# Kernel tuning notes

Hardware: AMD Instinct MI355X
Metric: run time of the kernel (lower is better)

The kernel has to match this reference:

```python
import jax, jax.numpy as jnp
import numpy as np

N_QUBIT = 20
N_LAYER = 50
FEAT = 128
BATCH = 128
N_NODES = BATCH * N_QUBIT * (N_LAYER + 1)  # 130560
N_EDGES = 524288
VOCAB = N_QUBIT * (N_LAYER + 1) + 1  # 1021
NEG_SLOPE = 0.01


def setup_inputs() -> dict:
    key = jax.random.key(0)
    ks = jax.random.split(key, 32)
    s = 0.05
    x = jax.random.randint(ks[0], (N_NODES,), 0, VOCAB, dtype=jnp.int64 if jax.config.read('jax_enable_x64') else jnp.int32)
    edge_index = jax.random.randint(ks[1], (2, N_EDGES), 0, N_NODES, dtype=x.dtype)
    emb = (jax.random.normal(ks[2], (VOCAB, FEAT), jnp.float32) * s).at[0].set(0.0)  # padding_idx=0
    gcn_w = jax.random.normal(ks[3], (5, FEAT, FEAT), jnp.float32) * s
    gcn_b = jnp.zeros((5, FEAT), jnp.float32)
    mlp_dims = [(2 * FEAT, 2 * FEAT), (2 * FEAT, FEAT), (FEAT, FEAT), (FEAT, FEAT // 2), (FEAT // 2, FEAT // 2), (FEAT // 2, 1)]
    mlp = {}
    for i, (din, dout) in enumerate(mlp_dims):
        mlp[f'mw{i}'] = jax.random.normal(ks[4 + i], (din, dout), jnp.float32) * s
        mlp[f'mb{i}'] = jnp.zeros((dout,), jnp.float32)
    return dict(x=x, edge_index=edge_index, emb=emb, gcn_w=gcn_w, gcn_b=gcn_b, **mlp)


def _leaky(v):
    return jnp.where(v >= 0, v, NEG_SLOPE * v)


def _gcn(h, src, dst, W, b):
    # PyG GCNConv: h' = D^-1/2 (A+I) D^-1/2 (h W) + b, flow src -> dst
    n = h.shape[0]
    hw = h @ W
    loops = jnp.arange(n, dtype=src.dtype)
    s2 = jnp.concatenate([src, loops])
    d2 = jnp.concatenate([dst, loops])
    deg = jax.ops.segment_sum(jnp.ones(s2.shape[0], hw.dtype), d2, num_segments=n)
    dinv = jnp.where(deg > 0, jax.lax.rsqrt(deg), 0.0)
    norm = dinv[s2] * dinv[d2]  # [E+N]
    out = jax.ops.segment_sum(hw[s2] * norm[:, None], d2, num_segments=n)
    return out + b


def reference(x, edge_index, emb, gcn_w, gcn_b, mw0, mb0, mw1, mb1, mw2, mb2, mw3, mb3, mw4, mb4, mw5, mb5):
    src, dst = edge_index[0], edge_index[1]
    h = emb[x]  # [N, f]
    for i in range(4):
        h = _leaky(_gcn(h, src, dst, gcn_w[i], gcn_b[i])) + h
    h = _gcn(h, src, dst, gcn_w[4], gcn_b[4]) + h
    n, f = N_QUBIT, FEAT
    h = h.reshape(-1, n * (N_LAYER + 1), f)[:, :n, :]  # [B, n, f]
    b = h.shape[0]
    # cartesian pairs (i, j): concat(h_i, h_j) -> [B, n, n, 2f]
    xi = jnp.broadcast_to(h[:, :, None, :], (b, n, n, f))
    xj = jnp.broadcast_to(h[:, None, :, :], (b, n, n, f))
    p = jnp.concatenate([xi, xj], axis=-1)
    p = _leaky(p @ mw0 + mb0)
    p = _leaky(p @ mw1 + mb1)
    p = _leaky(p @ mw2 + mb2)
    p = _leaky(p @ mw3 + mb3)
    p = _leaky(p @ mw4 + mb4)
    p = (p @ mw5 + mb5)[..., 0]  # [B, n, n]
    p = (p + jnp.swapaxes(p, -1, -2)) / 2
    return p.reshape(-1, n * n)
```

## Files before the change

kernel.cpp:

```cpp
#include <hip/hip_runtime.h>
#include <hip/hip_bf16.h>

#define NQ 20
#define NLAY 51
#define FEAT 128
#define BATCH 128
#define NN (BATCH * NQ * NLAY)
#define NE 524288
#define NPAIR (BATCH * NQ * NQ)
#define NB (NN / 256)
#define VOCAB 1021

typedef _Float16 half8 __attribute__((ext_vector_type(8)));
typedef float floatx4 __attribute__((ext_vector_type(4)));
typedef unsigned int uint;

__device__ __forceinline__ float lrelu(float v) { return v >= 0.f ? v : 0.01f * v; }

__device__ __forceinline__ uint packhl(float v) {
    _Float16 h = (_Float16)v;
    _Float16 l = (_Float16)(v - (float)h);
    union { _Float16 f; unsigned short u; } hb, lb;
    hb.f = h; lb.f = l;
    return (uint)hb.u | ((uint)lb.u << 16);
}

__device__ __forceinline__ void unpack8(uint4 a, uint4 b, half8& hi, half8& lo) {
    union { uint u[4]; half8 h; } H, L;
    H.u[0] = __builtin_amdgcn_perm(a.y, a.x, 0x05040100u);
    H.u[1] = __builtin_amdgcn_perm(a.w, a.z, 0x05040100u);
    H.u[2] = __builtin_amdgcn_perm(b.y, b.x, 0x05040100u);
    H.u[3] = __builtin_amdgcn_perm(b.w, b.z, 0x05040100u);
    L.u[0] = __builtin_amdgcn_perm(a.y, a.x, 0x07060302u);
    L.u[1] = __builtin_amdgcn_perm(a.w, a.z, 0x07060302u);
    L.u[2] = __builtin_amdgcn_perm(b.y, b.x, 0x07060302u);
    L.u[3] = __builtin_amdgcn_perm(b.w, b.z, 0x07060302u);
    hi = H.h;
    lo = L.h;
}

__global__ void k_count(const int* __restrict__ dst, int* __restrict__ cnt) {
    int e = blockIdx.x * 256 + threadIdx.x;
    atomicAdd(&cnt[dst[e]], 1);
}

__global__ void k_offsets(const int* __restrict__ cnt, const int* __restrict__ x,
                          int* __restrict__ offs, float* __restrict__ dinv,
                          int4* __restrict__ meta, int* __restrict__ cursor,
                          int* __restrict__ flag1, int* __restrict__ idmap) {
    __shared__ int sm[256];
    __shared__ int sbase;
    int t = threadIdx.x, g = blockIdx.x * 256 + t;
    int v = cnt[g];
    sm[t] = v;
    __syncthreads();
    for (int s = 1; s < 256; s <<= 1) {
        int add = (t >= s) ? sm[t - s] : 0;
        __syncthreads();
        sm[t] += add;
        __syncthreads();
    }
    if (t == 255) sbase = atomicAdd(cursor, sm[255]);
    __syncthreads();
    int off = sbase + sm[t] - v;
    float di = rsqrtf((float)(v + 1));
    offs[g] = off;
    dinv[g] = di;
    meta[g] = make_int4(off, v, __float_as_int(di), x[g]);
    if (g % (NQ * NLAY) < NQ) flag1[g] = 1;
    if (g < 1024) idmap[g] = min(g, VOCAB - 1);
}

__global__ void k_fill(const int* __restrict__ src, const int* __restrict__ dst,
                       const int* __restrict__ offs, int* __restrict__ fill,
                       const float* __restrict__ dinv, const int* __restrict__ x,
                       int2* __restrict__ csre, int2* __restrict__ csre0,
                       int* __restrict__ flag1) {
    int e = blockIdx.x * 256 + threadIdx.x;
    int d = dst[e];
    int s = src[e];
    int pos = offs[d] + atomicAdd(&fill[d], 1);
    int wb = __float_as_int(dinv[s] * dinv[d]);
    csre[pos] = make_int2(s, wb);
    csre0[pos] = make_int2(x[s], wb);
    if (d % (NQ * NLAY) < NQ) flag1[s] = 1;
}

__global__ void k_s1pass(const int* __restrict__ flagI, const int4* __restrict__ meta,
                         const int2* __restrict__ csre, int* __restrict__ cur,
                         int4* __restrict__ recO, int* __restrict__ flagO) {
    __shared__ int sm[256];
    __shared__ int sbase;
    int t = threadIdx.x, g = blockIdx.x * 256 + t;
    int v = flagI[g];
    sm[t] = v;
    __syncthreads();
    for (int s = 1; s < 256; s <<= 1) {
        int add = (t >= s) ? sm[t - s] : 0;
        __syncthreads();
        sm[t] += add;
        __syncthreads();
    }
    if (t == 255) sbase = atomicAdd(cur, sm[255]);
    __syncthreads();
    if (v) {
        int slot = sbase + sm[t] - 1;
        int4 m = meta[g];
        float di = __int_as_float(m.z);
        int dc = min(m.y, 6);
        int2 eb[6];
#pragma unroll
        for (int j = 0; j < 6; j++) eb[j] = (j < dc) ? csre[m.x + j] : make_int2(0, 0);
        int4* r = recO + (size_t)slot * 4;
        r[0] = make_int4(g + 1, m.y, __float_as_int(di * di), m.x);
        r[1] = make_int4(eb[0].x, eb[0].y, eb[1].x, eb[1].y);
        r[2] = make_int4(eb[2].x, eb[2].y, eb[3].x, eb[3].y);
        r[3] = make_int4(eb[4].x, eb[4].y, eb[5].x, eb[5].y);
        if (flagO) {
            flagO[g] = 1;
            for (int e = 0; e < m.y; e++) flagO[csre[m.x + e].x] = 1;
        }
    }
}

__global__ void k_rec0(const int4* __restrict__ meta, const int2* __restrict__ csre,
                       int4* __restrict__ rec0) {
    int q = blockIdx.x * 256 + threadIdx.x;
    if (q >= BATCH * NQ) return;
    int b = q / NQ, i = q - b * NQ;
    int node = b * (NQ * NLAY) + i;
    int4 m = meta[node];
    float di = __int_as_float(m.z);
    int dc = min(m.y, 6);
    int2 eb[6];
#pragma unroll
    for (int j = 0; j < 6; j++) eb[j] = (j < dc) ? csre[m.x + j] : make_int2(0, 0);
    int4* r = rec0 + (size_t)q * 4;
    r[0] = make_int4(node + 1, m.y, __float_as_int(di * di), m.x);
    r[1] = make_int4(eb[0].x, eb[0].y, eb[1].x, eb[1].y);
    r[2] = make_int4(eb[2].x, eb[2].y, eb[3].x, eb[3].y);
    r[3] = make_int4(eb[4].x, eb[4].y, eb[5].x, eb[5].y);
}

#define OFF_GCN 0
#define OFF_P0  81920
#define OFF_M1  147456
#define OFF_M2  180224
#define OFF_M3  196608
#define OFF_M4  204800
#define TS_TOTAL 208896

__global__ void k_tsplit_all(const float* __restrict__ gw, const float* __restrict__ mw0,
                             const float* __restrict__ mw1, const float* __restrict__ mw2,
                             const float* __restrict__ mw3, const float* __restrict__ mw4,
                             _Float16* __restrict__ hi, _Float16* __restrict__ lo) {
    int idx = blockIdx.x * 256 + threadIdx.x;
    const float* src;
    int K, N, rel;
    bool p0 = false;
    if (idx < OFF_P0) {
        int L = (idx - OFF_GCN) >> 14; rel = (idx - OFF_GCN) & 16383;
        src = gw + L * 16384; K = 128; N = 128;
    } else if (idx < OFF_M1) {
        rel = idx - OFF_P0; src = mw0; K = 128; N = 512; p0 = true;
    } else if (idx < OFF_M2) {
        rel = idx - OFF_M1;  src = mw1; K = 256; N = 128;
    } else if (idx < OFF_M3) {
        rel = idx - OFF_M2;  src = mw2; K = 128; N = 128;
    } else if (idx < OFF_M4) {
        rel = idx - OFF_M3;  src = mw3; K = 128; N = 64;
    } else {
        rel = idx - OFF_M4;  src = mw4; K = 64;  N = 64;
    }
    int kblks = K >> 5;
    int j = rel & 7;
    int lane = (rel >> 3) & 63;
    int t2 = rel >> 9;
    int kblk = t2 % kblks;
    int ntile = t2 / kblks;
    int col = ntile * 16 + (lane & 15);
    int k = kblk * 32 + ((lane >> 4) << 3) + j;
    float f;
    if (p0) {
        f = (col < 256) ? src[k * 256 + col] : src[(k + 128) * 256 + (col - 256)];
    } else {
        f = src[k * N + col];
    }
    _Float16 h = (_Float16)f;
    hi[idx] = h;
    lo[idx] = (_Float16)(f - (float)h);
}

template <int NT_N, bool LEAKY, bool BIAS, bool P0SPLIT, bool FUSEA, bool GATHA, bool LISTM>
__launch_bounds__(256, 2)
__global__ void hgemm(const float* __restrict__ A,
                      const float* __restrict__ FA, const float* __restrict__ FB,
                      const _Float16* __restrict__ Bh, const _Float16* __restrict__ Bl,
                      const float* __restrict__ bias,
                      float* __restrict__ C, float* __restrict__ C2,
                      int N, int K, const int* __restrict__ gmap,
                      const int* __restrict__ listm) {
    if (LISTM) {
        if ((unsigned)listm[blockIdx.x * 128] >= (unsigned)NN) return;
    }
    const int KB = K >> 5;
    const int lane = threadIdx.x & 63;
    const int wid = threadIdx.x >> 6;
    const int lm = lane & 15, lq = lane >> 4;
    const int m0 = blockIdx.x * 128 + wid * 32;
    const int n0t = blockIdx.y * NT_N;

    const float* arow[2];
    const float* brow[2];
#pragma unroll
    for (int mt = 0; mt < 2; mt++) {
        int row = m0 + mt * 16 + lm;
        if (FUSEA) {
            int b = row / (NQ * NQ);
            int rr = row - b * (NQ * NQ);
            int i = rr / NQ;
            int j = rr - i * NQ;
            arow[mt] = FA + (size_t)(b * NQ + i) * 256;
            brow[mt] = FB + (size_t)(b * NQ + j) * 256;
        } else if (GATHA) {
            arow[mt] = A + (size_t)gmap[row] * K;
        } else if (LISTM) {
            int lr = listm[row];
            lr = ((unsigned)lr < (unsigned)NN) ? lr : 0;
            arow[mt] = A + (size_t)lr * K;
        } else {
            arow[mt] = A + (size_t)row * K;
        }
    }

    floatx4 acc[2][NT_N];
#pragma unroll
    for (int mt = 0; mt < 2; mt++)
#pragma unroll
        for (int nt = 0; nt < NT_N; nt++) acc[mt][nt] = (floatx4)0.f;

    for (int kb = 0; kb < KB; kb++) {
        const int k0 = kb * 32 + lq * 8;
        half8 ahi[2], alo[2];
#pragma unroll
        for (int mt = 0; mt < 2; mt++) {
            floatx4 av0, av1;
            if (FUSEA) {
                floatx4 fa0 = *(const floatx4*)(arow[mt] + k0);
                floatx4 fa1 = *(const floatx4*)(arow[mt] + k0 + 4);
                floatx4 fb0 = *(const floatx4*)(brow[mt] + k0);
                floatx4 fb1 = *(const floatx4*)(brow[mt] + k0 + 4);
#pragma unroll
                for (int q = 0; q < 4; q++) {
                    av0[q] = lrelu(fa0[q] + fb0[q]);
                    av1[q] = lrelu(fa1[q] + fb1[q]);
                }
            } else {
                av0 = *(const floatx4*)(arow[mt] + k0);
                av1 = *(const floatx4*)(arow[mt] + k0 + 4);
            }
#pragma unroll
            for (int q = 0; q < 4; q++) {
                _Float16 h0 = (_Float16)av0[q];
                ahi[mt][q] = h0;
                alo[mt][q] = (_Float16)(av0[q] - (float)h0);
                _Float16 h1 = (_Float16)av1[q];
                ahi[mt][4 + q] = h1;
                alo[mt][4 + q] = (_Float16)(av1[q] - (float)h1);
            }
        }
#pragma unroll
        for (int nt = 0; nt < NT_N; nt++) {
            size_t boff = (((size_t)(n0t + nt) * KB + kb) * 64 + lane) * 8;
            half8 bhi = *(const half8*)(Bh + boff);
            half8 blo = *(const half8*)(Bl + boff);
#pragma unroll
            for (int mt = 0; mt < 2; mt++) {
                acc[mt][nt] = __builtin_amdgcn_mfma_f32_16x16x32_f16(ahi[mt], bhi, acc[mt][nt], 0, 0, 0);
                acc[mt][nt] = __builtin_amdgcn_mfma_f32_16x16x32_f16(ahi[mt], blo, acc[mt][nt], 0, 0, 0);
                acc[mt][nt] = __builtin_amdgcn_mfma_f32_16x16x32_f16(alo[mt], bhi, acc[mt][nt], 0, 0, 0);
            }
        }
    }

    int strow[2][4];
    bool svalid[2][4];
#pragma unroll
    for (int mt = 0; mt < 2; mt++)
#pragma unroll
        for (int r = 0; r < 4; r++) {
            int mlog = m0 + mt * 16 + lq * 4 + r;
            if (LISTM) {
                int sr = listm[mlog];
                svalid[mt][r] = (unsigned)sr < (unsigned)NN;
                strow[mt][r] = svalid[mt][r] ? sr : 0;
            } else {
                svalid[mt][r] = true;
                strow[mt][r] = mlog;
            }
        }

#pragma unroll
    for (int nt = 0; nt < NT_N; nt++) {
        int col = (n0t + nt) * 16 + lm;
        float bv = (BIAS || P0SPLIT) ? bias[col < 256 ? col : 0] : 0.f;
#pragma unroll
        for (int mt = 0; mt < 2; mt++) {
#pragma unroll
            for (int r = 0; r < 4; r++) {
                if (!svalid[mt][r]) continue;
                int row = strow[mt][r];
                float val = acc[mt][nt][r];
                if (P0SPLIT) {
                    if (col < 256) C[(size_t)row * 256 + col] = val + bv;
                    else C2[(size_t)row * 256 + col - 256] = val;
                } else {
                    if (BIAS) val += bv;
                    if (LEAKY) val = lrelu(val);
                    C[(size_t)row * N + col] = val;
                }
            }
        }
    }
}

template <bool LEAKY, bool FINAL>
__launch_bounds__(256, 8)
__global__ void k_lagg(const float* __restrict__ in, float* __restrict__ outp,
                       const int4* __restrict__ rec, const int2* __restrict__ csre,
                       const int* __restrict__ cntp, int fixcnt,
                       const _Float16* __restrict__ Bh, const _Float16* __restrict__ Bl,
                       const float* __restrict__ bias) {
    int lcnt = cntp ? *cntp : fixcnt;
    int sbase = blockIdx.x * 16;
    if (sbase >= lcnt) return;
    __shared__ uint X[16][132];
    __shared__ float R[16][132];
    __shared__ int NID[16];
    int tid = threadIdx.x;
    int sl = tid & 31;
    int grp = tid >> 5;
    const float4* in4 = (const float4*)in;
    {
        int lrow0 = grp * 2;
        int p0i = sbase + lrow0, p1i = p0i + 1;
        bool val0 = p0i < lcnt, val1 = p1i < lcnt;
        const int4* r0p = rec + (size_t)(val0 ? p0i : 0) * 4;
        const int4* r1p = rec + (size_t)(val1 ? p1i : 0) * 4;
        int4 hd0 = r0p[0], ea0 = r0p[1], eb0 = r0p[2], ec0 = r0p[3];
        int4 hd1 = r1p[0], ea1 = r1p[1], eb1 = r1p[2], ec1 = r1p[3];
        int n0 = hd0.x - 1;
        int n1 = hd1.x - 1;
        if (sl == 0) {
            NID[lrow0] = n0;
            NID[lrow0 + 1] = n1;
        }
        float s20 = __int_as_float(hd0.z), s21 = __int_as_float(hd1.z);
        float4 v0  = in4[(size_t)n0 * 32 + sl];
        float4 v1  = in4[(size_t)n1 * 32 + sl];
        float4 u00 = in4[(size_t)ea0.x * 32 + sl];
        float4 u01 = in4[(size_t)ea0.z * 32 + sl];
        float4 u02 = in4[(size_t)eb0.x * 32 + sl];
        float4 u03 = in4[(size_t)eb0.z * 32 + sl];
        float4 u04 = in4[(size_t)ec0.x * 32 + sl];
        float4 u05 = in4[(size_t)ec0.z * 32 + sl];
        float4 u10 = in4[(size_t)ea1.x * 32 + sl];
        float4 u11 = in4[(size_t)ea1.z * 32 + sl];
        float4 u12 = in4[(size_t)eb1.x * 32 + sl];
        float4 u13 = in4[(size_t)eb1.z * 32 + sl];
        float4 u14 = in4[(size_t)ec1.x * 32 + sl];
        float4 u15 = in4[(size_t)ec1.z * 32 + sl];
        *(float4*)&R[lrow0][sl * 4] = v0;
        *(float4*)&R[lrow0 + 1][sl * 4] = v1;
        float w00 = __int_as_float(ea0.y), w01 = __int_as_float(ea0.w);
        float w02 = __int_as_float(eb0.y), w03 = __int_as_float(eb0.w);
        float w04 = __int_as_float(ec0.y), w05 = __int_as_float(ec0.w);
        float w10 = __int_as_float(ea1.y), w11 = __int_as_float(ea1.w);
        float w12 = __int_as_float(eb1.y), w13 = __int_as_float(eb1.w);
        float w14 = __int_as_float(ec1.y), w15 = __int_as_float(ec1.w);
        float a0x = v0.x * s20 + u00.x * w00 + u01.x * w01 + u02.x * w02 + u03.x * w03 + u04.x * w04 + u05.x * w05;
        float a0y = v0.y * s20 + u00.y * w00 + u01.y * w01 + u02.y * w02 + u03.y * w03 + u04.y * w04 + u05.y * w05;
        float a0z = v0.z * s20 + u00.z * w00 + u01.z * w01 + u02.z * w02 + u03.z * w03 + u04.z * w04 + u05.z * w05;
        float a0w = v0.w * s20 + u00.w * w00 + u01.w * w01 + u02.w * w02 + u03.w * w03 + u04.w * w04 + u05.w * w05;
        float a1x = v1.x * s21 + u10.x * w10 + u11.x * w11 + u12.x * w12 + u13.x * w13 + u14.x * w14 + u15.x * w15;
        float a1y = v1.y * s21 + u10.y * w10 + u11.y * w11 + u12.y * w12 + u13.y * w13 + u14.y * w14 + u15.y * w15;
        float a1z = v1.z * s21 + u10.z * w10 + u11.z * w11 + u12.z * w12 + u13.z * w13 + u14.z * w14 + u15.z * w15;
        float a1w = v1.w * s21 + u10.w * w10 + u11.w * w11 + u12.w * w12 + u13.w * w13 + u14.w * w14 + u15.w * w15;
        int deg0 = val0 ? hd0.y : 0, deg1 = val1 ? hd1.y : 0;
        int dm = max(deg0, deg1);
        if (dm > 6) {
            int off0 = hd0.w, off1 = hd1.w;
            int d0c = max(deg0 - 1, 0), d1c = max(deg1 - 1, 0);
            for (int e = 6; e < dm; e += 6) {
                int2 e00 = csre[off0 + min(e,     d0c)];
                int2 e01 = csre[off0 + min(e + 1, d0c)];
                int2 e02 = csre[off0 + min(e + 2, d0c)];
                int2 e03 = csre[off0 + min(e + 3, d0c)];
                int2 e04 = csre[off0 + min(e + 4, d0c)];
                int2 e05 = csre[off0 + min(e + 5, d0c)];
                int2 e10 = csre[off1 + min(e,     d1c)];
                int2 e11 = csre[off1 + min(e + 1, d1c)];
                int2 e12 = csre[off1 + min(e + 2, d1c)];
                int2 e13 = csre[off1 + min(e + 3, d1c)];
                int2 e14 = csre[off1 + min(e + 4, d1c)];
                int2 e15 = csre[off1 + min(e + 5, d1c)];
                float4 x00 = in4[(size_t)e00.x * 32 + sl];
                float4 x01 = in4[(size_t)e01.x * 32 + sl];
                float4 x02 = in4[(size_t)e02.x * 32 + sl];
                float4 x03 = in4[(size_t)e03.x * 32 + sl];
                float4 x04 = in4[(size_t)e04.x * 32 + sl];
                float4 x05 = in4[(size_t)e05.x * 32 + sl];
                float4 x10 = in4[(size_t)e10.x * 32 + sl];
                float4 x11 = in4[(size_t)e11.x * 32 + sl];
                float4 x12 = in4[(size_t)e12.x * 32 + sl];
                float4 x13 = in4[(size_t)e13.x * 32 + sl];
                float4 x14 = in4[(size_t)e14.x * 32 + sl];
                float4 x15 = in4[(size_t)e15.x * 32 + sl];
                float q00 = (e     < deg0) ? __int_as_float(e00.y) : 0.f;
                float q01 = (e + 1 < deg0) ? __int_as_float(e01.y) : 0.f;
                float q02 = (e + 2 < deg0) ? __int_as_float(e02.y) : 0.f;
                float q03 = (e + 3 < deg0) ? __int_as_float(e03.y) : 0.f;
                float q04 = (e + 4 < deg0) ? __int_as_float(e04.y) : 0.f;
                float q05 = (e + 5 < deg0) ? __int_as_float(e05.y) : 0.f;
                float q10 = (e     < deg1) ? __int_as_float(e10.y) : 0.f;
                float q11 = (e + 1 < deg1) ? __int_as_float(e11.y) : 0.f;
                float q12 = (e + 2 < deg1) ? __int_as_float(e12.y) : 0.f;
                float q13 = (e + 3 < deg1) ? __int_as_float(e13.y) : 0.f;
                float q14 = (e + 4 < deg1) ? __int_as_float(e14.y) : 0.f;
                float q15 = (e + 5 < deg1) ? __int_as_float(e15.y) : 0.f;
                a0x += x00.x * q00 + x01.x * q01 + x02.x * q02 + x03.x * q03 + x04.x * q04 + x05.x * q05;
                a0y += x00.y * q00 + x01.y * q01 + x02.y * q02 + x03.y * q03 + x04.y * q04 + x05.y * q05;
                a0z += x00.z * q00 + x01.z * q01 + x02.z * q02 + x03.z * q03 + x04.z * q04 + x05.z * q05;
                a0w += x00.w * q00 + x01.w * q01 + x02.w * q02 + x03.w * q03 + x04.w * q04 + x05.w * q05;
                a1x += x10.x * q10 + x11.x * q11 + x12.x * q12 + x13.x * q13 + x14.x * q14 + x15.x * q15;
                a1y += x10.y * q10 + x11.y * q11 + x12.y * q12 + x13.y * q13 + x14.y * q14 + x15.y * q15;
                a1z += x10.z * q10 + x11.z * q11 + x12.z * q12 + x13.z * q13 + x14.z * q14 + x15.z * q15;
                a1w += x10.w * q10 + x11.w * q11 + x12.w * q12 + x13.w * q13 + x14.w * q14 + x15.w * q15;
            }
        }
        *(uint4*)&X[lrow0][sl * 4] =
            make_uint4(packhl(a0x), packhl(a0y), packhl(a0z), packhl(a0w));
        *(uint4*)&X[lrow0 + 1][sl * 4] =
            make_uint4(packhl(a1x), packhl(a1y), packhl(a1z), packhl(a1w));
    }
    __syncthreads();
    const int lane = tid & 63;
    const int wid = tid >> 6;
    const int lm = lane & 15, lq = lane >> 4;
    floatx4 acc[2];
    acc[0] = (floatx4)0.f;
    acc[1] = (floatx4)0.f;
#pragma unroll
    for (int kb = 0; kb < 4; kb++) {
        const int k0 = kb * 32 + lq * 8;
        uint4 pa = *(const uint4*)&X[lm][k0];
        uint4 pb = *(const uint4*)&X[lm][k0 + 4];
        half8 ahi, alo;
        unpack8(pa, pb, ahi, alo);
#pragma unroll
        for (int ntl = 0; ntl < 2; ntl++) {
            int nt = wid * 2 + ntl;
            size_t boff = (((size_t)nt * 4 + kb) * 64 + lane) * 8;
            half8 bhi = *(const half8*)(Bh + boff);
            half8 blo = *(const half8*)(Bl + boff);
            acc[ntl] = __builtin_amdgcn_mfma_f32_16x16x32_f16(ahi, bhi, acc[ntl], 0, 0, 0);
            acc[ntl] = __builtin_amdgcn_mfma_f32_16x16x32_f16(ahi, blo, acc[ntl], 0, 0, 0);
            acc[ntl] = __builtin_amdgcn_mfma_f32_16x16x32_f16(alo, bhi, acc[ntl], 0, 0, 0);
        }
    }
    int nodes[4];
    bool sval[4];
#pragma unroll
    for (int r = 0; r < 4; r++) {
        int slot = sbase + lq * 4 + r;
        sval[r] = slot < lcnt;
        nodes[r] = NID[lq * 4 + r];
    }
#pragma unroll
    for (int ntl = 0; ntl < 2; ntl++) {
        int col = (wid * 2 + ntl) * 16 + lm;
        float bv = bias[col];
#pragma unroll
        for (int r = 0; r < 4; r++) {
            if (!sval[r]) continue;
            float val = acc[ntl][r] + bv;
            if (LEAKY) val = lrelu(val);
            val += R[lq * 4 + r][col];
            if (FINAL)
                outp[(size_t)(sbase + lq * 4 + r) * FEAT + col] = val;
            else
                outp[(size_t)nodes[r] * FEAT + col] = val;
        }
    }
}

template <int KB, int NT>
__device__ __forceinline__ void pair_stage(uint (*__restrict__ X)[132],
                                           const _Float16* __restrict__ Bh,
                                           const _Float16* __restrict__ Bl,
                                           const float* __restrict__ bias,
                                           int srow, int lane) {
    const int lm = lane & 15, lq = lane >> 4;
    floatx4 acc[NT];
#pragma unroll
    for (int nt = 0; nt < NT; nt++) acc[nt] = (floatx4)0.f;
#pragma unroll
    for (int kb = 0; kb < KB; kb++) {
        const int k0 = kb * 32 + lq * 8;
        uint4 pa = *(const uint4*)&X[srow + lm][k0];
        uint4 pb = *(const uint4*)&X[srow + lm][k0 + 4];
        half8 ahi, alo;
        unpack8(pa, pb, ahi, alo);
#pragma unroll
        for (int nt = 0; nt < NT; nt++) {
            size_t boff = (((size_t)nt * KB + kb) * 64 + lane) * 8;
            half8 bhi = *(const half8*)(Bh + boff);
            half8 blo = *(const half8*)(Bl + boff);
            acc[nt] = __builtin_amdgcn_mfma_f32_16x16x32_f16(ahi, bhi, acc[nt], 0, 0, 0);
            acc[nt] = __builtin_amdgcn_mfma_f32_16x16x32_f16(ahi, blo, acc[nt], 0, 0, 0);
            acc[nt] = __builtin_amdgcn_mfma_f32_16x16x32_f16(alo, bhi, acc[nt], 0, 0, 0);
        }
    }
#pragma unroll
    for (int nt = 0; nt < NT; nt++) {
        int col = nt * 16 + lm;
        float bv = bias[col];
#pragma unroll
        for (int r = 0; r < 4; r++) {
            X[srow + lq * 4 + r][col] = packhl(lrelu(acc[nt][r] + bv));
        }
    }
}

__launch_bounds__(256, 4)
__global__ void k_pair(const float* __restrict__ FA, const float* __restrict__ FB,
                       const _Float16* __restrict__ bth, const _Float16* __restrict__ btl,
                       const float* __restrict__ mb1, const float* __restrict__ mb2,
                       const float* __restrict__ mb3, const float* __restrict__ mb4,
                       const float* __restrict__ mw5, const float* __restrict__ mb5,
                       float* __restrict__ sbuf) {
    __shared__ uint X[64][132];
    const int lane = threadIdx.x & 63;
    const int wid = threadIdx.x >> 6;
    const int lm = lane & 15, lq = lane >> 4;
    const int srow = wid * 16;
    const int rbase = blockIdx.x * 64;

    {
        const int grow = rbase + srow + lm;
        int b = grow / (NQ * NQ);
        int rr = grow - b * (NQ * NQ);
        int i = rr / NQ;
        int j = rr - i * NQ;
        const float* arow = FA + (size_t)(b * NQ + i) * 256;
        const float* brow = FB + (size_t)(b * NQ + j) * 256;
        const _Float16* Bh = bth + OFF_M1;
        const _Float16* Bl = btl + OFF_M1;
        floatx4 acc[8];
#pragma unroll
        for (int nt = 0; nt < 8; nt++) acc[nt] = (floatx4)0.f;
        const int KB = 8;
#pragma unroll
        for (int kb = 0; kb < KB; kb++) {
            const int k0 = kb * 32 + lq * 8;
            floatx4 fa0 = *(const floatx4*)(arow + k0);
            floatx4 fa1 = *(const floatx4*)(arow + k0 + 4);
            floatx4 fb0 = *(const floatx4*)(brow + k0);
            floatx4 fb1 = *(const floatx4*)(brow + k0 + 4);
            half8 ahi, alo;
#pragma unroll
            for (int q = 0; q < 4; q++) {
                float v0 = lrelu(fa0[q] + fb0[q]);
                float v1 = lrelu(fa1[q] + fb1[q]);
                _Float16 h0 = (_Float16)v0;
                ahi[q] = h0;
                alo[q] = (_Float16)(v0 - (float)h0);
                _Float16 h1 = (_Float16)v1;
                ahi[4 + q] = h1;
                alo[4 + q] = (_Float16)(v1 - (float)h1);
            }
#pragma unroll
            for (int nt = 0; nt < 8; nt++) {
                size_t boff = (((size_t)nt * KB + kb) * 64 + lane) * 8;
                half8 bhi = *(const half8*)(Bh + boff);
                half8 blo = *(const half8*)(Bl + boff);
                acc[nt] = __builtin_amdgcn_mfma_f32_16x16x32_f16(ahi, bhi, acc[nt], 0, 0, 0);
                acc[nt] = __builtin_amdgcn_mfma_f32_16x16x32_f16(ahi, blo, acc[nt], 0, 0, 0);
                acc[nt] = __builtin_amdgcn_mfma_f32_16x16x32_f16(alo, bhi, acc[nt], 0, 0, 0);
            }
        }
#pragma unroll
        for (int nt = 0; nt < 8; nt++) {
            int col = nt * 16 + lm;
            float bv = mb1[col];
#pragma unroll
            for (int r = 0; r < 4; r++) {
                X[srow + lq * 4 + r][col] = packhl(lrelu(acc[nt][r] + bv));
            }
        }
    }
    pair_stage<4, 8>(X, bth + OFF_M2, btl + OFF_M2, mb2, srow, lane);
    pair_stage<4, 4>(X, bth + OFF_M3, btl + OFF_M3, mb3, srow, lane);
    pair_stage<2, 4>(X, bth + OFF_M4, btl + OFF_M4, mb4, srow, lane);
    {
        int row = srow + (lane >> 2);
        int part = lane & 3;
        float s = 0.f;
#pragma unroll
        for (int c4 = 0; c4 < 4; c4++) {
            int c0 = part * 16 + c4 * 4;
            uint4 u = *(const uint4*)&X[row][c0];
            const float* wp = mw5 + c0;
            uint uu[4] = {u.x, u.y, u.z, u.w};
#pragma unroll
            for (int q = 0; q < 4; q++) {
                union { unsigned short us; _Float16 f; } ch, cl;
                ch.us = (unsigned short)(uu[q] & 0xffffu);
                cl.us = (unsigned short)(uu[q] >> 16);
                s += ((float)ch.f + (float)cl.f) * wp[q];
            }
        }
        s += __shfl_xor(s, 1);
        s += __shfl_xor(s, 2);
        if (part == 0) sbuf[rbase + row] = s + mb5[0];
    }
}

__global__ void k_sym(const float* __restrict__ sbuf, float* __restrict__ out) {
    int p = blockIdx.x * 256 + threadIdx.x;
    int b = p / (NQ * NQ);
    int rr = p - b * (NQ * NQ);
    int i = rr / NQ, j = rr - i * NQ;
    float a = sbuf[p];
    float c = sbuf[b * (NQ * NQ) + j * NQ + i];
    out[p] = 0.5f * (a + c);
}

__global__ void k_agg0(const float* __restrict__ embW, const float* __restrict__ emb,
                       float* __restrict__ h,
                       const int4* __restrict__ meta, const int2* __restrict__ csre0,
                       const float* __restrict__ bias) {
    int tid = threadIdx.x;
    int sl = tid & 31;
    int p = blockIdx.x * 8 + (tid >> 5);
    int n0 = p * 2, n1 = n0 + 1;
    int4 m0 = meta[n0], m1 = meta[n1];
    float di0 = __int_as_float(m0.z), di1 = __int_as_float(m1.z);
    int off0 = m0.x, deg0 = m0.y;
    int off1 = m1.x, deg1 = m1.y;
    float4 v0 = ((const float4*)(embW + (size_t)m0.w * FEAT))[sl];
    float4 v1 = ((const float4*)(embW + (size_t)m1.w * FEAT))[sl];
    float4 ho0 = ((const float4*)(emb + (size_t)m0.w * FEAT))[sl];
    float4 ho1 = ((const float4*)(emb + (size_t)m1.w * FEAT))[sl];
    float s20 = di0 * di0, s21 = di1 * di1;
    float a0x = v0.x * s20, a0y = v0.y * s20, a0z = v0.z * s20, a0w = v0.w * s20;
    float a1x = v1.x * s21, a1y = v1.y * s21, a1z = v1.z * s21, a1w = v1.w * s21;
    int d0c = max(deg0 - 1, 0), d1c = max(deg1 - 1, 0);
    int dm = max(deg0, deg1);
    for (int e = 0; e < dm; e += 4) {
        int2 e00 = csre0[off0 + min(e,     d0c)];
        int2 e01 = csre0[off0 + min(e + 1, d0c)];
        int2 e02 = csre0[off0 + min(e + 2, d0c)];
        int2 e03 = csre0[off0 + min(e + 3, d0c)];
        int2 e10 = csre0[off1 + min(e,     d1c)];
        int2 e11 = csre0[off1 + min(e + 1, d1c)];
        int2 e12 = csre0[off1 + min(e + 2, d1c)];
        int2 e13 = csre0[off1 + min(e + 3, d1c)];
        float4 u00 = ((const float4*)(embW + (size_t)e00.x * FEAT))[sl];
        float4 u01 = ((const float4*)(embW + (size_t)e01.x * FEAT))[sl];
        float4 u02 = ((const float4*)(embW + (size_t)e02.x * FEAT))[sl];
        float4 u03 = ((const float4*)(embW + (size_t)e03.x * FEAT))[sl];
        float4 u10 = ((const float4*)(embW + (size_t)e10.x * FEAT))[sl];
        float4 u11 = ((const float4*)(embW + (size_t)e11.x * FEAT))[sl];
        float4 u12 = ((const float4*)(embW + (size_t)e12.x * FEAT))[sl];
        float4 u13 = ((const float4*)(embW + (size_t)e13.x * FEAT))[sl];
        float w00 = (e     < deg0) ? __int_as_float(e00.y) : 0.f;
        float w01 = (e + 1 < deg0) ? __int_as_float(e01.y) : 0.f;
        float w02 = (e + 2 < deg0) ? __int_as_float(e02.y) : 0.f;
        float w03 = (e + 3 < deg0) ? __int_as_float(e03.y) : 0.f;
        float w10 = (e     < deg1) ? __int_as_float(e10.y) : 0.f;
        float w11 = (e + 1 < deg1) ? __int_as_float(e11.y) : 0.f;
        float w12 = (e + 2 < deg1) ? __int_as_float(e12.y) : 0.f;
        float w13 = (e + 3 < deg1) ? __int_as_float(e13.y) : 0.f;
        a0x += u00.x * w00 + u01.x * w01 + u02.x * w02 + u03.x * w03;
        a0y += u00.y * w00 + u01.y * w01 + u02.y * w02 + u03.y * w03;
        a0z += u00.z * w00 + u01.z * w01 + u02.z * w02 + u03.z * w03;
        a0w += u00.w * w00 + u01.w * w01 + u02.w * w02 + u03.w * w03;
        a1x += u10.x * w10 + u11.x * w11 + u12.x * w12 + u13.x * w13;
        a1y += u10.y * w10 + u11.y * w11 + u12.y * w12 + u13.y * w13;
        a1z += u10.z * w10 + u11.z * w11 + u12.z * w12 + u13.z * w13;
        a1w += u10.w * w10 + u11.w * w11 + u12.w * w12 + u13.w * w13;
    }
    float4 bv = ((const float4*)bias)[sl];
    float4 r0, r1;
    r0.x = lrelu(a0x + bv.x) + ho0.x;
    r0.y = lrelu(a0y + bv.y) + ho0.y;
    r0.z = lrelu(a0z + bv.z) + ho0.z;
    r0.w = lrelu(a0w + bv.w) + ho0.w;
    r1.x = lrelu(a1x + bv.x) + ho1.x;
    r1.y = lrelu(a1y + bv.y) + ho1.y;
    r1.z = lrelu(a1z + bv.z) + ho1.z;
    r1.w = lrelu(a1w + bv.w) + ho1.w;
    ((float4*)(h + (size_t)n0 * FEAT))[sl] = r0;
    ((float4*)(h + (size_t)n1 * FEAT))[sl] = r1;
}

extern "C" void kernel_launch(void* const* d_in, const int* in_sizes, int n_in,
                              void* d_out, int out_size, void* d_ws, size_t ws_size,
                              hipStream_t stream) {
    const int* x = (const int*)d_in[0];
    const int* ei = (const int*)d_in[1];
    const int* e_src = ei;
    const int* e_dst = ei + NE;
    const float* emb = (const float*)d_in[2];
    const float* gw = (const float*)d_in[3];
    const float* gb = (const float*)d_in[4];
    const float* mw0 = (const float*)d_in[5];
    const float* mb0 = (const float*)d_in[6];
    const float* mw1 = (const float*)d_in[7];
    const float* mb1 = (const float*)d_in[8];
    const float* mw2 = (const float*)d_in[9];
    const float* mb2 = (const float*)d_in[10];
    const float* mw3 = (const float*)d_in[11];
    const float* mb3 = (const float*)d_in[12];
    const float* mw4 = (const float*)d_in[13];
    const float* mb4 = (const float*)d_in[14];
    const float* mw5 = (const float*)d_in[15];
    const float* mb5 = (const float*)d_in[16];
    float* out = (float*)d_out;

    float* wsf = (float*)d_ws;
    size_t o = 0;
    const size_t HSZ = (size_t)NN * FEAT;
    float* h  = wsf + o; o += HSZ;
    float* hw = wsf + o; o += HSZ;
    int* cnt   = (int*)(wsf + o); o += NN;
    int* fill  = (int*)(wsf + o); o += NN;
    int* flag1 = (int*)(wsf + o); o += NN;
    int* flag2 = (int*)(wsf + o); o += NN;
    int* flag3 = (int*)(wsf + o); o += NN;
    int* curs  = (int*)(wsf + o); o += 16;
    int* offs = (int*)(wsf + o); o += NN;
    float* dinv = wsf + o; o += NN;
    int4* meta = (int4*)(wsf + o); o += 4 * (size_t)NN;
    int2* csre  = (int2*)(wsf + o); o += 2 * (size_t)(NE + 8);
    int2* csre0 = (int2*)(wsf + o); o += 2 * (size_t)(NE + 8);
    int* idmap = (int*)(wsf + o); o += 1024;
    float* embW = wsf + o; o += (size_t)1024 * FEAT;
    float* hq = wsf + o; o += (size_t)BATCH * NQ * FEAT;
    float* Abuf = wsf + o; o += (size_t)BATCH * NQ * 256;
    float* Bbuf = wsf + o; o += (size_t)BATCH * NQ * 256;
    int4* rec1 = (int4*)(wsf + o); o += 16 * (size_t)NN;
    int4* rec2 = (int4*)(wsf + o); o += 16 * (size_t)NN;
    int4* rec3 = (int4*)(wsf + o); o += 16 * (size_t)NN;
    int4* rec0 = (int4*)(wsf + o); o += 16 * (size_t)(BATCH * NQ);
    _Float16* bt_hi = (_Float16*)(wsf + o); o += (TS_TOTAL + 2) / 2;
    _Float16* bt_lo = (_Float16*)(wsf + o); o += (TS_TOTAL + 2) / 2;
    float* sbuf = hw;

    k_tsplit_all<<<TS_TOTAL / 256, 256, 0, stream>>>(gw, mw0, mw1, mw2, mw3, mw4, bt_hi, bt_lo);

    hipMemsetAsync(cnt, 0, (5 * NN + 16) * sizeof(int), stream);
    hipMemsetAsync(csre + NE, 0, 8 * sizeof(int2), stream);
    hipMemsetAsync(csre0 + NE, 0, 8 * sizeof(int2), stream);
    k_count<<<NE / 256, 256, 0, stream>>>(e_dst, cnt);
    k_offsets<<<NB, 256, 0, stream>>>(cnt, x, offs, dinv, meta, curs + 0, flag1, idmap);
    k_fill<<<NE / 256, 256, 0, stream>>>(e_src, e_dst, offs, fill, dinv, x, csre, csre0, flag1);
    k_rec0<<<(BATCH * NQ + 255) / 256, 256, 0, stream>>>(meta, csre, rec0);
    k_s1pass<<<NB, 256, 0, stream>>>(flag1, meta, csre, curs + 1, rec1, flag2);
    k_s1pass<<<NB, 256, 0, stream>>>(flag2, meta, csre, curs + 2, rec2, flag3);
    k_s1pass<<<NB, 256, 0, stream>>>(flag3, meta, csre, curs + 3, rec3, nullptr);

    hgemm<1, false, false, false, false, true, false><<<dim3(8, 8), 256, 0, stream>>>(
        emb, nullptr, nullptr, bt_hi + OFF_GCN, bt_lo + OFF_GCN,
        nullptr, embW, nullptr, FEAT, FEAT, idmap, nullptr);
    k_agg0<<<NN / 16, 256, 0, stream>>>(embW, emb, h, meta, csre0, gb + 0 * FEAT);

    k_lagg<true, false><<<NN / 16, 256, 0, stream>>>(
        h, hw, rec3, csre, curs + 3, 0,
        bt_hi + OFF_GCN + 1 * 16384, bt_lo + OFF_GCN + 1 * 16384, gb + 1 * FEAT);
    k_lagg<true, false><<<NN / 16, 256, 0, stream>>>(
        hw, h, rec2, csre, curs + 2, 0,
        bt_hi + OFF_GCN + 2 * 16384, bt_lo + OFF_GCN + 2 * 16384, gb + 2 * FEAT);
    k_lagg<true, false><<<NN / 16, 256, 0, stream>>>(
        h, hw, rec1, csre, curs + 1, 0,
        bt_hi + OFF_GCN + 3 * 16384, bt_lo + OFF_GCN + 3 * 16384, gb + 3 * FEAT);
    k_lagg<false, true><<<(BATCH * NQ) / 16, 256, 0, stream>>>(
        hw, hq, rec0, csre, nullptr, BATCH * NQ,
        bt_hi + OFF_GCN + 4 * 16384, bt_lo + OFF_GCN + 4 * 16384, gb + 4 * FEAT);

    hgemm<2, false, false, true, false, false, false><<<dim3(20, 16), 256, 0, stream>>>(
        hq, nullptr, nullptr, bt_hi + OFF_P0, bt_lo + OFF_P0, mb0, Abuf, Bbuf, 512, 128,
        nullptr, nullptr);
    k_pair<<<NPAIR / 64, 256, 0, stream>>>(Abuf, Bbuf, bt_hi, bt_lo,
                                           mb1, mb2, mb3, mb4, mw5, mb5, sbuf);
    k_sym<<<NPAIR / 256, 256, 0, stream>>>(sbuf, out);
}
```

Measured before the change: 390.1 us.

## Fuse rec0 build, pair-projection GEMM and symmetrization into neighbouring kernels

Folds the rec0 record construction into the first k_s1pass launch as extra blocks. Fuses the final GCN layer with the first MLP projection (hq @ mw0 split into A/B halves), keeping the tile in shared memory. Replaces k_sym with atomic adds from k_pair into a zeroed output. This removes three launches and the hq/sbuf round trips, at the cost of an output memset and two atomics per pair.

```diff
diff --git a/kernel.cpp b/kernel.cpp
--- a/kernel.cpp
+++ b/kernel.cpp
@@ -88,7 +88,27 @@
 
 __global__ void k_s1pass(const int* __restrict__ flagI, const int4* __restrict__ meta,
                          const int2* __restrict__ csre, int* __restrict__ cur,
-                         int4* __restrict__ recO, int* __restrict__ flagO) {
+                         int4* __restrict__ recO, int* __restrict__ flagO,
+                         int4* __restrict__ rec0q) {
+    if (rec0q && blockIdx.x >= NB) {
+        int q = (blockIdx.x - NB) * 256 + threadIdx.x;
+        if (q < BATCH * NQ) {
+            int b = q / NQ, i = q - b * NQ;
+            int node = b * (NQ * NLAY) + i;
+            int4 m = meta[node];
+            float di = __int_as_float(m.z);
+            int dc = min(m.y, 6);
+            int2 eb[6];
+#pragma unroll
+            for (int j = 0; j < 6; j++) eb[j] = (j < dc) ? csre[m.x + j] : make_int2(0, 0);
+            int4* r = rec0q + (size_t)q * 4;
+            r[0] = make_int4(node + 1, m.y, __float_as_int(di * di), m.x);
+            r[1] = make_int4(eb[0].x, eb[0].y, eb[1].x, eb[1].y);
+            r[2] = make_int4(eb[2].x, eb[2].y, eb[3].x, eb[3].y);
+            r[3] = make_int4(eb[4].x, eb[4].y, eb[5].x, eb[5].y);
+        }
+        return;
+    }
     __shared__ int sm[256];
     __shared__ int sbase;
     int t = threadIdx.x, g = blockIdx.x * 256 + t;
@@ -121,25 +141,6 @@
             for (int e = 0; e < m.y; e++) flagO[csre[m.x + e].x] = 1;
         }
     }
-}
-
-__global__ void k_rec0(const int4* __restrict__ meta, const int2* __restrict__ csre,
-                       int4* __restrict__ rec0) {
-    int q = blockIdx.x * 256 + threadIdx.x;
-    if (q >= BATCH * NQ) return;
-    int b = q / NQ, i = q - b * NQ;
-    int node = b * (NQ * NLAY) + i;
-    int4 m = meta[node];
-    float di = __int_as_float(m.z);
-    int dc = min(m.y, 6);
-    int2 eb[6];
-#pragma unroll
-    for (int j = 0; j < 6; j++) eb[j] = (j < dc) ? csre[m.x + j] : make_int2(0, 0);
-    int4* r = rec0 + (size_t)q * 4;
-    r[0] = make_int4(node + 1, m.y, __float_as_int(di * di), m.x);
-    r[1] = make_int4(eb[0].x, eb[0].y, eb[1].x, eb[1].y);
-    r[2] = make_int4(eb[2].x, eb[2].y, eb[3].x, eb[3].y);
-    r[3] = make_int4(eb[4].x, eb[4].y, eb[5].x, eb[5].y);
 }
 
 #define OFF_GCN 0
@@ -330,7 +331,10 @@
                        const int4* __restrict__ rec, const int2* __restrict__ csre,
                        const int* __restrict__ cntp, int fixcnt,
                        const _Float16* __restrict__ Bh, const _Float16* __restrict__ Bl,
-                       const float* __restrict__ bias) {
+                       const float* __restrict__ bias,
+                       const _Float16* __restrict__ BhP, const _Float16* __restrict__ BlP,
+                       const float* __restrict__ mb0p,
+                       float* __restrict__ Abuf, float* __restrict__ Bbuf) {
     int lcnt = cntp ? *cntp : fixcnt;
     int sbase = blockIdx.x * 16;
     if (sbase >= lcnt) return;
@@ -468,6 +472,7 @@
             acc[ntl] = __builtin_amdgcn_mfma_f32_16x16x32_f16(alo, bhi, acc[ntl], 0, 0, 0);
         }
     }
+    if (FINAL) __syncthreads();
     int nodes[4];
     bool sval[4];
 #pragma unroll
@@ -487,9 +492,48 @@
             if (LEAKY) val = lrelu(val);
             val += R[lq * 4 + r][col];
             if (FINAL)
-                outp[(size_t)(sbase + lq * 4 + r) * FEAT + col] = val;
+                X[lq * 4 + r][col] = packhl(val);
             else
                 outp[(size_t)nodes[r] * FEAT + col] = val;
+        }
+    }
+    if (FINAL) {
+        __syncthreads();
+#pragma unroll
+        for (int c = 0; c < 2; c++) {
+            floatx4 acc4[4];
+#pragma unroll
+            for (int nt = 0; nt < 4; nt++) acc4[nt] = (floatx4)0.f;
+#pragma unroll
+            for (int kb = 0; kb < 4; kb++) {
+                const int k0 = kb * 32 + lq * 8;
+                uint4 pa = *(const uint4*)&X[lm][k0];
+                uint4 pb = *(const uint4*)&X[lm][k0 + 4];
+                half8 ahi, alo;
+                unpack8(pa, pb, ahi, alo);
+#pragma unroll
+                for (int nt = 0; nt < 4; nt++) {
+                    int T = wid * 8 + c * 4 + nt;
+                    size_t boff = (((size_t)T * 4 + kb) * 64 + lane) * 8;
+                    half8 bhi = *(const half8*)(BhP + boff);
+                    half8 blo = *(const half8*)(BlP + boff);
+                    acc4[nt] = __builtin_amdgcn_mfma_f32_16x16x32_f16(ahi, bhi, acc4[nt], 0, 0, 0);
+                    acc4[nt] = __builtin_amdgcn_mfma_f32_16x16x32_f16(ahi, blo, acc4[nt], 0, 0, 0);
+                    acc4[nt] = __builtin_amdgcn_mfma_f32_16x16x32_f16(alo, bhi, acc4[nt], 0, 0, 0);
+                }
+            }
+#pragma unroll
+            for (int nt = 0; nt < 4; nt++) {
+                int T = wid * 8 + c * 4 + nt;
+                int col = T * 16 + lm;
+#pragma unroll
+                for (int r = 0; r < 4; r++) {
+                    int q = sbase + lq * 4 + r;
+                    float val = acc4[nt][r];
+                    if (col < 256) Abuf[(size_t)q * 256 + col] = val + mb0p[col];
+                    else Bbuf[(size_t)q * 256 + col - 256] = val;
+                }
+            }
         }
     }
 }
@@ -538,7 +582,7 @@
                        const float* __restrict__ mb1, const float* __restrict__ mb2,
                        const float* __restrict__ mb3, const float* __restrict__ mb4,
                        const float* __restrict__ mw5, const float* __restrict__ mb5,
-                       float* __restrict__ sbuf) {
+                       float* __restrict__ out) {
     __shared__ uint X[64][132];
     const int lane = threadIdx.x & 63;
     const int wid = threadIdx.x >> 6;
@@ -622,18 +666,16 @@
         }
         s += __shfl_xor(s, 1);
         s += __shfl_xor(s, 2);
-        if (part == 0) sbuf[rbase + row] = s + mb5[0];
-    }
-}
-
-__global__ void k_sym(const float* __restrict__ sbuf, float* __restrict__ out) {
-    int p = blockIdx.x * 256 + threadIdx.x;
-    int b = p / (NQ * NQ);
-    int rr = p - b * (NQ * NQ);
-    int i = rr / NQ, j = rr - i * NQ;
-    float a = sbuf[p];
-    float c = sbuf[b * (NQ * NQ) + j * NQ + i];
-    out[p] = 0.5f * (a + c);
+        if (part == 0) {
+            int p = rbase + row;
+            int b = p / (NQ * NQ);
+            int rr = p - b * (NQ * NQ);
+            int i = rr / NQ, j = rr - i * NQ;
+            float hv = 0.5f * (s + mb5[0]);
+            atomicAdd(&out[(size_t)b * NQ * NQ + i * NQ + j], hv);
+            atomicAdd(&out[(size_t)b * NQ * NQ + j * NQ + i], hv);
+        }
+    }
 }
 
 __global__ void k_agg0(const float* __restrict__ embW, const float* __restrict__ emb,
@@ -747,7 +789,6 @@
     int2* csre0 = (int2*)(wsf + o); o += 2 * (size_t)(NE + 8);
     int* idmap = (int*)(wsf + o); o += 1024;
     float* embW = wsf + o; o += (size_t)1024 * FEAT;
-    float* hq = wsf + o; o += (size_t)BATCH * NQ * FEAT;
     float* Abuf = wsf + o; o += (size_t)BATCH * NQ * 256;
     float* Bbuf = wsf + o; o += (size_t)BATCH * NQ * 256;
     int4* rec1 = (int4*)(wsf + o); o += 16 * (size_t)NN;
@@ -756,7 +797,8 @@
     int4* rec0 = (int4*)(wsf + o); o += 16 * (size_t)(BATCH * NQ);
     _Float16* bt_hi = (_Float16*)(wsf + o); o += (TS_TOTAL + 2) / 2;
     _Float16* bt_lo = (_Float16*)(wsf + o); o += (TS_TOTAL + 2) / 2;
-    float* sbuf = hw;
+
+    hipMemsetAsync(out, 0, (size_t)NPAIR * sizeof(float), stream);
 
     k_tsplit_all<<<TS_TOTAL / 256, 256, 0, stream>>>(gw, mw0, mw1, mw2, mw3, mw4, bt_hi, bt_lo);
 
@@ -766,10 +808,10 @@
     k_count<<<NE / 256, 256, 0, stream>>>(e_dst, cnt);
     k_offsets<<<NB, 256, 0, stream>>>(cnt, x, offs, dinv, meta, curs + 0, flag1, idmap);
     k_fill<<<NE / 256, 256, 0, stream>>>(e_src, e_dst, offs, fill, dinv, x, csre, csre0, flag1);
-    k_rec0<<<(BATCH * NQ + 255) / 256, 256, 0, stream>>>(meta, csre, rec0);
-    k_s1pass<<<NB, 256, 0, stream>>>(flag1, meta, csre, curs + 1, rec1, flag2);
-    k_s1pass<<<NB, 256, 0, stream>>>(flag2, meta, csre, curs + 2, rec2, flag3);
-    k_s1pass<<<NB, 256, 0, stream>>>(flag3, meta, csre, curs + 3, rec3, nullptr);
+    k_s1pass<<<NB + (BATCH * NQ + 255) / 256, 256, 0, stream>>>(
+        flag1, meta, csre, curs + 1, rec1, flag2, rec0);
+    k_s1pass<<<NB, 256, 0, stream>>>(flag2, meta, csre, curs + 2, rec2, flag3, nullptr);
+    k_s1pass<<<NB, 256, 0, stream>>>(flag3, meta, csre, curs + 3, rec3, nullptr, nullptr);
 
     hgemm<1, false, false, false, false, true, false><<<dim3(8, 8), 256, 0, stream>>>(
         emb, nullptr, nullptr, bt_hi + OFF_GCN, bt_lo + OFF_GCN,
@@ -778,21 +820,21 @@
 
     k_lagg<true, false><<<NN / 16, 256, 0, stream>>>(
         h, hw, rec3, csre, curs + 3, 0,
-        bt_hi + OFF_GCN + 1 * 16384, bt_lo + OFF_GCN + 1 * 16384, gb + 1 * FEAT);
+        bt_hi + OFF_GCN + 1 * 16384, bt_lo + OFF_GCN + 1 * 16384, gb + 1 * FEAT,
+        nullptr, nullptr, nullptr, nullptr, nullptr);
     k_lagg<true, false><<<NN / 16, 256, 0, stream>>>(
         hw, h, rec2, csre, curs + 2, 0,
-        bt_hi + OFF_GCN + 2 * 16384, bt_lo + OFF_GCN + 2 * 16384, gb + 2 * FEAT);
+        bt_hi + OFF_GCN + 2 * 16384, bt_lo + OFF_GCN + 2 * 16384, gb + 2 * FEAT,
+        nullptr, nullptr, nullptr, nullptr, nullptr);
     k_lagg<true, false><<<NN / 16, 256, 0, stream>>>(
         h, hw, rec1, csre, curs + 1, 0,
-        bt_hi + OFF_GCN + 3 * 16384, bt_lo + OFF_GCN + 3 * 16384, gb + 3 * FEAT);
+        bt_hi + OFF_GCN + 3 * 16384, bt_lo + OFF_GCN + 3 * 16384, gb + 3 * FEAT,
+        nullptr, nullptr, nullptr, nullptr, nullptr);
     k_lagg<false, true><<<(BATCH * NQ) / 16, 256, 0, stream>>>(
-        hw, hq, rec0, csre, nullptr, BATCH * NQ,
-        bt_hi + OFF_GCN + 4 * 16384, bt_lo + OFF_GCN + 4 * 16384, gb + 4 * FEAT);
-
-    hgemm<2, false, false, true, false, false, false><<<dim3(20, 16), 256, 0, stream>>>(
-        hq, nullptr, nullptr, bt_hi + OFF_P0, bt_lo + OFF_P0, mb0, Abuf, Bbuf, 512, 128,
-        nullptr, nullptr);
+        hw, nullptr, rec0, csre, nullptr, BATCH * NQ,
+        bt_hi + OFF_GCN + 4 * 16384, bt_lo + OFF_GCN + 4 * 16384, gb + 4 * FEAT,
+        bt_hi + OFF_P0, bt_lo + OFF_P0, mb0, Abuf, Bbuf);
+
     k_pair<<<NPAIR / 64, 256, 0, stream>>>(Abuf, Bbuf, bt_hi, bt_lo,
-                                           mb1, mb2, mb3, mb4, mw5, mb5, sbuf);
-    k_sym<<<NPAIR / 256, 256, 0, stream>>>(sbuf, out);
-}
+                                           mb1, mb2, mb3, mb4, mw5, mb5, out);
+}
```

After: 392.1 us. About the same (+0.5%).
